# Performance work log

Measured on AMD Instinct MI355X. Metric: run time of the kernel, lower is better.

## Reference

```python
import jax, jax.numpy as jnp
import numpy as np

N = 50000
E = 400000
IN_DIM = 128
HID = 128
OUT = 128
HEADS = 4
NEG_SLOPE = 0.2
EPS = 1e-16


def setup_inputs() -> dict:
    key = jax.random.key(0)
    ks = jax.random.split(key, 12)
    s = 0.05
    return {
        "x": jax.random.normal(ks[0], (N, IN_DIM), dtype=jnp.float32),
        "edge_index": jax.random.randint(ks[1], (2, E), 0, N, dtype=jnp.int64),
        # layer 1: in_dim -> hid, heads=4, concat
        "W1": jax.random.normal(ks[2], (IN_DIM, HEADS * HID), dtype=jnp.float32) * s,
        "att_src1": jax.random.normal(ks[3], (HEADS, HID), dtype=jnp.float32) * s,
        "att_dst1": jax.random.normal(ks[4], (HEADS, HID), dtype=jnp.float32) * s,
        "bias1": jnp.zeros((HEADS * HID,), dtype=jnp.float32),
        # layer 2: hid*heads -> out, heads=1, no concat
        "W2": jax.random.normal(ks[5], (HEADS * HID, OUT), dtype=jnp.float32) * s,
        "att_src2": jax.random.normal(ks[6], (1, OUT), dtype=jnp.float32) * s,
        "att_dst2": jax.random.normal(ks[7], (1, OUT), dtype=jnp.float32) * s,
        "bias2": jnp.zeros((OUT,), dtype=jnp.float32),
    }


def gat_conv(x, src, dst, W, att_src, att_dst, bias, heads, out_dim, concat):
    n = x.shape[0]
    h = (x @ W).reshape(n, heads, out_dim)                       # [N,H,D]
    a_src = jnp.sum(h * att_src[None], axis=-1)                  # [N,H]
    a_dst = jnp.sum(h * att_dst[None], axis=-1)                  # [N,H]
    e = jax.nn.leaky_relu(a_src[src] + a_dst[dst], NEG_SLOPE)    # [E,H]
    # segment softmax over incoming edges of each dst node
    e_max = jax.ops.segment_max(e, dst, num_segments=n)          # [N,H]
    ex = jnp.exp(e - e_max[dst])
    denom = jax.ops.segment_sum(ex, dst, num_segments=n)         # [N,H]
    alpha = ex / (denom[dst] + EPS)                              # [E,H]
    msg = h[src] * alpha[..., None]                              # [E,H,D]
    out = jax.ops.segment_sum(msg, dst, num_segments=n)          # [N,H,D]
    out = out.reshape(n, heads * out_dim) if concat else out.mean(axis=1)
    return out + bias


def reference(x, edge_index, W1, att_src1, att_dst1, bias1, W2, att_src2, att_dst2, bias2):
    n = x.shape[0]
    loop = jnp.arange(n, dtype=edge_index.dtype)
    src = jnp.concatenate([edge_index[0], loop])  # PyG add_self_loops=True
    dst = jnp.concatenate([edge_index[1], loop])
    h = jax.nn.elu(gat_conv(x, src, dst, W1, att_src1, att_dst1, bias1, HEADS, HID, True))
    z = jax.nn.elu(gat_conv(h, src, dst, W2, att_src2, att_dst2, bias2, 1, OUT, False))
    # F.normalize(z, dim=-1): L2 with eps=1e-12 clamp on the norm
    norm = jnp.maximum(jnp.linalg.norm(z, axis=-1, keepdims=True), 1e-12)
    return z / norm
```

## Files before the change

kernel.cpp:

```cpp
#include <hip/hip_runtime.h>
#include <cstddef>

#define N_NODES 50000
#define N_EDGES 400000
#define TOT_EDGES (N_EDGES + N_NODES)
#define M_PAD 50048
#define SCAN_PAD 50176
#define NBLK 49

typedef _Float16 f16;
typedef __attribute__((ext_vector_type(8))) _Float16 f16x8;
typedef __attribute__((ext_vector_type(4))) _Float16 f16x4;
typedef __attribute__((ext_vector_type(2))) _Float16 f16x2;
typedef __attribute__((ext_vector_type(4))) float f32x4;

__global__ void zero_int(int* __restrict__ p, int n) {
  int i = blockIdx.x * blockDim.x + threadIdx.x;
  if (i < n) p[i] = 0;
}

__global__ void count_kernel(const int* __restrict__ ei, int* __restrict__ deg) {
  int e = blockIdx.x * blockDim.x + threadIdx.x;
  if (e >= TOT_EDGES) return;
  int dst = (e < N_EDGES) ? ei[N_EDGES + e] : (e - N_EDGES);
  atomicAdd(&deg[dst], 1);
}

__global__ __launch_bounds__(256) void blk_hist(const int* __restrict__ deg,
                                                int* __restrict__ blkcnt) {
  __shared__ int lh[128];
  const int t = threadIdx.x;
  if (t < 128) lh[t] = 0;
  __syncthreads();
  const int base = blockIdx.x * 1024;
#pragma unroll
  for (int j = 0; j < 4; ++j) {
    const int i = base + j * 256 + t;
    if (i < N_NODES) atomicAdd(&lh[min(deg[i], 127)], 1);
  }
  __syncthreads();
  if (t < 128) blkcnt[t * NBLK + blockIdx.x] = lh[t];
}

__global__ __launch_bounds__(128) void sort_scan(const int* __restrict__ blkcnt,
                                                 int* __restrict__ boff) {
  __shared__ int tot[128];
  const int t = threadIdx.x;
  int s = 0;
  for (int k = 0; k < NBLK; ++k) s += blkcnt[t * NBLK + k];
  tot[t] = s;
  __syncthreads();
  if (t == 0) {
    int acc = 0;
    for (int b = 0; b < 128; ++b) { const int v = tot[b]; tot[b] = acc; acc += v; }
  }
  __syncthreads();
  int acc = tot[t];
  for (int k = 0; k < NBLK; ++k) {
    const int v = blkcnt[t * NBLK + k];
    boff[t * NBLK + k] = acc;
    acc += v;
  }
}

__global__ __launch_bounds__(256) void scatter2(const int* __restrict__ deg,
                                                const int* __restrict__ boff,
                                                int* __restrict__ order) {
  __shared__ int lcur[128];
  const int t = threadIdx.x;
  if (t < 128) lcur[t] = boff[t * NBLK + blockIdx.x];
  __syncthreads();
  const int base = blockIdx.x * 1024;
#pragma unroll
  for (int j = 0; j < 4; ++j) {
    const int i = base + j * 256 + t;
    if (i < N_NODES) {
      const int b = min(deg[i], 127);
      const int pos = atomicAdd(&lcur[b], 1);
      order[pos] = i;
    }
  }
}

__global__ __launch_bounds__(256) void block_scan(const int* __restrict__ cnt,
                                                  int* __restrict__ pre,
                                                  int* __restrict__ bsum) {
  __shared__ int wsum[4];
  const int t = threadIdx.x, lane = t & 63, w = t >> 6;
  const int base = blockIdx.x * 1024 + t * 4;
  int4 v = *(const int4*)&cnt[base];
  const int s = v.x + v.y + v.z + v.w;
  int x = s;
#pragma unroll
  for (int off = 1; off < 64; off <<= 1) {
    int y = __shfl_up(x, off);
    if (lane >= off) x += y;
  }
  if (lane == 63) wsum[w] = x;
  __syncthreads();
  int woff = 0;
  for (int j = 0; j < w; ++j) woff += wsum[j];
  const int ex = x - s + woff;
  pre[base + 0] = ex;
  pre[base + 1] = ex + v.x;
  pre[base + 2] = ex + v.x + v.y;
  pre[base + 3] = ex + v.x + v.y + v.z;
  if (t == 255) bsum[blockIdx.x] = ex + s;
}

__global__ void bsum_scan(int* __restrict__ bsum, int nb) {
  const int lane = threadIdx.x;
  int v = (lane < nb) ? bsum[lane] : 0;
  int x = v;
#pragma unroll
  for (int off = 1; off < 64; off <<= 1) {
    int y = __shfl_up(x, off);
    if (lane >= off) x += y;
  }
  if (lane < nb) bsum[lane] = x - v;
}

__global__ __launch_bounds__(256) void add_off(int* __restrict__ pre,
                                               const int* __restrict__ boff,
                                               int* __restrict__ cursor) {
  const int base = blockIdx.x * 1024 + threadIdx.x * 4;
  const int off = boff[blockIdx.x];
  int4 v = *(const int4*)&pre[base];
  v.x += off; v.y += off; v.z += off; v.w += off;
  *(int4*)&pre[base] = v;
  *(int4*)&cursor[base] = v;
}

__global__ void fill_kernel(const int* __restrict__ ei, int* __restrict__ cursor,
                            int* __restrict__ csr_src) {
  int e = blockIdx.x * blockDim.x + threadIdx.x;
  if (e >= TOT_EDGES) return;
  int s, d;
  if (e < N_EDGES) { s = ei[e]; d = ei[N_EDGES + e]; }
  else             { s = d = e - N_EDGES; }
  int pos = atomicAdd(&cursor[d], 1);
  csr_src[pos] = s;
}

__global__ __launch_bounds__(256) void prep_x(const float* __restrict__ x,
                                              f16* __restrict__ xb,
                                              const float* __restrict__ V1s,
                                              const float* __restrict__ V1d,
                                              float* __restrict__ as1,
                                              float* __restrict__ ad1,
                                              f16* __restrict__ aggb) {
  const int wid = (blockIdx.x * 256 + threadIdx.x) >> 6;
  const int lane = threadIdx.x & 63;
  if (wid >= M_PAD) return;
  const int k = lane * 2;
  if (wid >= N_NODES) {
    f16x2 z; z[0] = (f16)0.f; z[1] = (f16)0.f;
    *(f16x2*)&xb[(size_t)wid * 128 + k] = z;
    f16x8 z8;
#pragma unroll
    for (int j = 0; j < 8; ++j) z8[j] = (f16)0.f;
    *(f16x8*)&aggb[(size_t)wid * 512 + lane * 8] = z8;
    return;
  }
  float2 xv = *(const float2*)&x[(size_t)wid * 128 + k];
  f16x2 o; o[0] = (f16)xv.x; o[1] = (f16)xv.y;
  *(f16x2*)&xb[(size_t)wid * 128 + k] = o;

  float4 vs0 = *(const float4*)&V1s[k * 4];
  float4 vs1 = *(const float4*)&V1s[(k + 1) * 4];
  float4 vd0 = *(const float4*)&V1d[k * 4];
  float4 vd1 = *(const float4*)&V1d[(k + 1) * 4];
  float s[4], d[4];
  s[0] = xv.x * vs0.x + xv.y * vs1.x;
  s[1] = xv.x * vs0.y + xv.y * vs1.y;
  s[2] = xv.x * vs0.z + xv.y * vs1.z;
  s[3] = xv.x * vs0.w + xv.y * vs1.w;
  d[0] = xv.x * vd0.x + xv.y * vd1.x;
  d[1] = xv.x * vd0.y + xv.y * vd1.y;
  d[2] = xv.x * vd0.z + xv.y * vd1.z;
  d[3] = xv.x * vd0.w + xv.y * vd1.w;
#pragma unroll
  for (int h = 0; h < 4; ++h) {
#pragma unroll
    for (int off = 32; off; off >>= 1) {
      s[h] += __shfl_xor(s[h], off);
      d[h] += __shfl_xor(d[h], off);
    }
  }
  if (lane == 0) {
    *(float4*)&as1[(size_t)wid * 4] = make_float4(s[0], s[1], s[2], s[3]);
    *(float4*)&ad1[(size_t)wid * 4] = make_float4(d[0], d[1], d[2], d[3]);
  }
}

__global__ __launch_bounds__(256) void prep_weights(
    const float* __restrict__ W1, const float* __restrict__ W2,
    const float* __restrict__ att_s1, const float* __restrict__ att_d1,
    const float* __restrict__ att_s2, const float* __restrict__ att_d2,
    f16* __restrict__ w1t, f16* __restrict__ w2t,
    float* __restrict__ V1s, float* __restrict__ V1d,
    float* __restrict__ V2s, float* __restrict__ V2d) {
  const int b = blockIdx.x;
  if (b < 256) {
    const int idx = b * 256 + threadIdx.x;
    const int cc = idx >> 7, rr = idx & 127;
    w1t[idx] = (f16)W1[(size_t)rr * 512 + cc];
  } else if (b < 512) {
    const int idx = (b - 256) * 256 + threadIdx.x;
    const int cc = idx >> 9, rr = idx & 511;
    w2t[idx] = (f16)W2[(size_t)rr * 128 + cc];
  } else if (b < 640) {
    const int wid = (b - 512) * 4 + (threadIdx.x >> 6);
    const int lane = threadIdx.x & 63;
    const int k = wid >> 2, h = wid & 3;
    const float* wrow = W1 + (size_t)k * 512 + h * 128;
    float2 wv = *(const float2*)&wrow[lane * 2];
    float2 sv = *(const float2*)&att_s1[h * 128 + lane * 2];
    float2 dv = *(const float2*)&att_d1[h * 128 + lane * 2];
    float ps = wv.x * sv.x + wv.y * sv.y;
    float pd = wv.x * dv.x + wv.y * dv.y;
#pragma unroll
    for (int off = 32; off; off >>= 1) {
      ps += __shfl_xor(ps, off);
      pd += __shfl_xor(pd, off);
    }
    if (lane == 0) { V1s[k * 4 + h] = ps; V1d[k * 4 + h] = pd; }
  } else {
    const int wid = (b - 640) * 4 + (threadIdx.x >> 6);
    const int lane = threadIdx.x & 63;
    const float* wrow = W2 + (size_t)wid * 128;
    float2 wv = *(const float2*)&wrow[lane * 2];
    float2 sv = *(const float2*)&att_s2[lane * 2];
    float2 dv = *(const float2*)&att_d2[lane * 2];
    float ps = wv.x * sv.x + wv.y * sv.y;
    float pd = wv.x * dv.x + wv.y * dv.y;
#pragma unroll
    for (int off = 32; off; off >>= 1) {
      ps += __shfl_xor(ps, off);
      pd += __shfl_xor(pd, off);
    }
    if (lane == 0) { V2s[wid] = ps; V2d[wid] = pd; }
  }
}

template <int K, bool PER_HEAD, bool FUSE_A2>
__global__ __launch_bounds__(256) void gemm_bt(const f16* __restrict__ A, int lda,
                                               const f16* __restrict__ Bt, int ldb,
                                               f16* __restrict__ C, int ldc,
                                               const float* __restrict__ bias,
                                               const float* __restrict__ V2s,
                                               const float* __restrict__ V2d,
                                               float* __restrict__ as2,
                                               float* __restrict__ ad2) {
  if constexpr (PER_HEAD) {
    const int hh = blockIdx.y;
    A += (size_t)hh * 128;
    Bt += (size_t)hh * 128 * 128;
    C += (size_t)hh * 128;
    bias += hh * 128;
  }
  constexpr int LDT = 40;
  __shared__ __align__(16) f16 As[128 * LDT];
  __shared__ __align__(16) f16 Bs[128 * LDT];
  const int tid = threadIdx.x;
  const int lane = tid & 63;
  const int g = lane >> 4, r16 = lane & 15;
  const int w = tid >> 6, wr = w >> 1, wc = w & 1;
  const long bm = (long)blockIdx.x * 128;

  const int row0 = tid >> 2, h0 = tid & 3;
  const int p1 = (h0 & 1) * 16 + (h0 >> 1) * 4;
  const size_t ga0 = (size_t)(bm + row0) * lda + h0 * 8;
  const size_t ga1 = (size_t)(bm + row0 + 64) * lda + h0 * 8;
  const size_t gb0 = (size_t)row0 * ldb + h0 * 8;
  const size_t gb1 = (size_t)(row0 + 64) * ldb + h0 * 8;
  const int la0 = row0 * LDT + p1, la1 = (row0 + 64) * LDT + p1;

  f32x4 acc[4][4] = {};
  float s2a = 0.f, d2a = 0.f, s2b = 0.f, d2b = 0.f;

  for (int k0 = 0; k0 < K; k0 += 32) {
    __syncthreads();
    f16x8 va0 = *(const f16x8*)&A[ga0 + k0];
    f16x8 va1 = *(const f16x8*)&A[ga1 + k0];
    f16x8 vb0 = *(const f16x8*)&Bt[gb0 + k0];
    f16x8 vb1 = *(const f16x8*)&Bt[gb1 + k0];
    if constexpr (FUSE_A2) {
      const int kc = k0 + h0 * 8;
      float4 vsa = *(const float4*)&V2s[kc];
      float4 vsb = *(const float4*)&V2s[kc + 4];
      float4 vda = *(const float4*)&V2d[kc];
      float4 vdb = *(const float4*)&V2d[kc + 4];
      const float vs[8] = {vsa.x, vsa.y, vsa.z, vsa.w, vsb.x, vsb.y, vsb.z, vsb.w};
      const float vd[8] = {vda.x, vda.y, vda.z, vda.w, vdb.x, vdb.y, vdb.z, vdb.w};
#pragma unroll
      for (int j = 0; j < 8; ++j) {
        s2a += (float)va0[j] * vs[j];
        d2a += (float)va0[j] * vd[j];
        s2b += (float)va1[j] * vs[j];
        d2b += (float)va1[j] * vd[j];
      }
    }
    *(f16x4*)&As[la0]     = __builtin_shufflevector(va0, va0, 0, 1, 2, 3);
    *(f16x4*)&As[la0 + 8] = __builtin_shufflevector(va0, va0, 4, 5, 6, 7);
    *(f16x4*)&As[la1]     = __builtin_shufflevector(va1, va1, 0, 1, 2, 3);
    *(f16x4*)&As[la1 + 8] = __builtin_shufflevector(va1, va1, 4, 5, 6, 7);
    *(f16x4*)&Bs[la0]     = __builtin_shufflevector(vb0, vb0, 0, 1, 2, 3);
    *(f16x4*)&Bs[la0 + 8] = __builtin_shufflevector(vb0, vb0, 4, 5, 6, 7);
    *(f16x4*)&Bs[la1]     = __builtin_shufflevector(vb1, vb1, 0, 1, 2, 3);
    *(f16x4*)&Bs[la1 + 8] = __builtin_shufflevector(vb1, vb1, 4, 5, 6, 7);
    __syncthreads();
    f16x8 af[4], bfv[4];
#pragma unroll
    for (int m = 0; m < 4; ++m)
      af[m] = *(const f16x8*)&As[(wr * 64 + m * 16 + r16) * LDT + g * 8];
#pragma unroll
    for (int n = 0; n < 4; ++n)
      bfv[n] = *(const f16x8*)&Bs[(wc * 64 + n * 16 + r16) * LDT + g * 8];
#pragma unroll
    for (int m = 0; m < 4; ++m)
#pragma unroll
      for (int n = 0; n < 4; ++n)
        acc[m][n] = __builtin_amdgcn_mfma_f32_16x16x32_f16(af[m], bfv[n], acc[m][n], 0, 0, 0);
  }

  if constexpr (FUSE_A2) {
    s2a += __shfl_xor(s2a, 1); s2a += __shfl_xor(s2a, 2);
    d2a += __shfl_xor(d2a, 1); d2a += __shfl_xor(d2a, 2);
    s2b += __shfl_xor(s2b, 1); s2b += __shfl_xor(s2b, 2);
    d2b += __shfl_xor(d2b, 1); d2b += __shfl_xor(d2b, 2);
    if ((tid & 3) == 0) {
      const long r0 = bm + row0;
      as2[r0] = s2a; ad2[r0] = d2a;
      as2[r0 + 64] = s2b; ad2[r0 + 64] = d2b;
    }
  }

#pragma unroll
  for (int m = 0; m < 4; ++m) {
#pragma unroll
    for (int n = 0; n < 4; ++n) {
      const long row = bm + wr * 64 + m * 16 + g * 4;
      const int col = wc * 64 + n * 16 + r16;
      float bv = 0.f;
      if constexpr (PER_HEAD) bv = bias[col];
#pragma unroll
      for (int r = 0; r < 4; ++r) {
        float v = acc[m][n][r];
        if constexpr (PER_HEAD) {
          v += bv;
          v = v > 0.f ? v : (__expf(v) - 1.f);
        }
        C[(size_t)(row + r) * ldc + col] = (f16)v;
      }
    }
  }
}

__global__ __launch_bounds__(256) void aggregate1x(
    const f16* __restrict__ xsrc, const float* __restrict__ a_src,
    const float* __restrict__ a_dst, const int* __restrict__ rowstart,
    const int* __restrict__ csr, const int* __restrict__ order,
    f16* __restrict__ aggb) {
  const int wave = (blockIdx.x * blockDim.x + threadIdx.x) >> 6;
  const int lane = threadIdx.x & 63;
  const int g16 = lane >> 4, l16 = lane & 15;
  const int node = order[wave * 4 + g16];
  const int col0 = l16 * 8;
  const int rs = rowstart[node];
  const int re = rowstart[node + 1];
  const int deg = re - rs;
  float4 adv = *(const float4*)&a_dst[(size_t)node * 4];

  int maxdeg = deg;
  maxdeg = max(maxdeg, __shfl_xor(maxdeg, 16));
  maxdeg = max(maxdeg, __shfl_xor(maxdeg, 32));

  constexpr int D = 4;
  int sreg[D];
  float4 areg[D];
  f16x8 hreg[D];
#pragma unroll
  for (int p = 0; p < D; ++p) {
    const int k = rs + p;
    const int s = csr[(k < re) ? k : (re - 1)];
    areg[p] = *(const float4*)&a_src[(size_t)s * 4];
    hreg[p] = *(const f16x8*)&xsrc[(size_t)s * 128 + col0];
    const int k2 = rs + D + p;
    sreg[p] = csr[(k2 < re) ? k2 : (re - 1)];
  }

  float acc0[8] = {}, acc1[8] = {}, acc2[8] = {}, acc3[8] = {};
  float Z0 = 0.f, Z1 = 0.f, Z2 = 0.f, Z3 = 0.f;
  for (int base = 0; base < maxdeg; base += D) {
#pragma unroll
    for (int p = 0; p < D; ++p) {
      const int i = base + p;
      const bool act = i < deg;
      float4 av = areg[p];
      float e0 = av.x + adv.x; e0 = e0 > 0.f ? e0 : 0.2f * e0;
      float e1 = av.y + adv.y; e1 = e1 > 0.f ? e1 : 0.2f * e1;
      float e2 = av.z + adv.z; e2 = e2 > 0.f ? e2 : 0.2f * e2;
      float e3 = av.w + adv.w; e3 = e3 > 0.f ? e3 : 0.2f * e3;
      const float w0 = act ? __expf(e0) : 0.f;
      const float w1 = act ? __expf(e1) : 0.f;
      const float w2 = act ? __expf(e2) : 0.f;
      const float w3 = act ? __expf(e3) : 0.f;
      const f16x8 h = hreg[p];
      const int nk = rs + i + D;
      if (nk < re) {
        const int s = sreg[p];
        areg[p] = *(const float4*)&a_src[(size_t)s * 4];
        hreg[p] = *(const f16x8*)&xsrc[(size_t)s * 128 + col0];
      }
      const int nk2 = rs + i + 2 * D;
      if (nk2 < re) sreg[p] = csr[nk2];
      Z0 += w0; Z1 += w1; Z2 += w2; Z3 += w3;
#pragma unroll
      for (int j = 0; j < 8; ++j) {
        const float hv = (float)h[j];
        acc0[j] += w0 * hv;
        acc1[j] += w1 * hv;
        acc2[j] += w2 * hv;
        acc3[j] += w3 * hv;
      }
    }
  }

  const float i0 = 1.f / (Z0 + 1e-16f);
  const float i1 = 1.f / (Z1 + 1e-16f);
  const float i2 = 1.f / (Z2 + 1e-16f);
  const float i3 = 1.f / (Z3 + 1e-16f);
  f16* orow = aggb + (size_t)node * 512 + col0;
  f16x8 o0, o1, o2, o3;
#pragma unroll
  for (int j = 0; j < 8; ++j) {
    o0[j] = (f16)(acc0[j] * i0);
    o1[j] = (f16)(acc1[j] * i1);
    o2[j] = (f16)(acc2[j] * i2);
    o3[j] = (f16)(acc3[j] * i3);
  }
  *(f16x8*)&orow[0]   = o0;
  *(f16x8*)&orow[128] = o1;
  *(f16x8*)&orow[256] = o2;
  *(f16x8*)&orow[384] = o3;
}

__global__ __launch_bounds__(256) void aggregate2(
    const f16* __restrict__ hsrc, const float* __restrict__ a_src,
    const float* __restrict__ a_dst, const int* __restrict__ rowstart,
    const int* __restrict__ csr, const int* __restrict__ order,
    const float* __restrict__ bias, float* __restrict__ out) {
  const int wave = (blockIdx.x * blockDim.x + threadIdx.x) >> 6;
  const int lane = threadIdx.x & 63;
  const int g16 = lane >> 4, l16 = lane & 15;
  const int node = order[wave * 4 + g16];
  const int col0 = l16 * 8;
  const int rs = rowstart[node];
  const int re = rowstart[node + 1];
  const int deg = re - rs;
  const float ad = a_dst[node];

  int maxdeg = deg;
  maxdeg = max(maxdeg, __shfl_xor(maxdeg, 16));
  maxdeg = max(maxdeg, __shfl_xor(maxdeg, 32));

  constexpr int D = 6;
  int sreg[D];
  float areg[D];
  f16x8 hreg[D];
#pragma unroll
  for (int p = 0; p < D; ++p) {
    const int k = rs + p;
    const int s = csr[(k < re) ? k : (re - 1)];
    areg[p] = a_src[s];
    hreg[p] = *(const f16x8*)&hsrc[(size_t)s * 128 + col0];
    const int k2 = rs + D + p;
    sreg[p] = csr[(k2 < re) ? k2 : (re - 1)];
  }

  float acc[8] = {};
  float Z = 0.f;
  for (int base = 0; base < maxdeg; base += D) {
#pragma unroll
    for (int p = 0; p < D; ++p) {
      const int i = base + p;
      const bool act = i < deg;
      float e = areg[p] + ad;
      e = e > 0.f ? e : 0.2f * e;
      const float w = act ? __expf(e) : 0.f;
      const f16x8 h = hreg[p];
      const int nk = rs + i + D;
      if (nk < re) {
        const int s = sreg[p];
        areg[p] = a_src[s];
        hreg[p] = *(const f16x8*)&hsrc[(size_t)s * 128 + col0];
      }
      const int nk2 = rs + i + 2 * D;
      if (nk2 < re) sreg[p] = csr[nk2];
      Z += w;
#pragma unroll
      for (int j = 0; j < 8; ++j) acc[j] += w * (float)h[j];
    }
  }
  const float inv = 1.f / (Z + 1e-16f);

  float4 ba = *(const float4*)&bias[col0];
  float4 bb = *(const float4*)&bias[col0 + 4];
  const float bv[8] = {ba.x, ba.y, ba.z, ba.w, bb.x, bb.y, bb.z, bb.w};
  float v[8];
  float ss = 0.f;
#pragma unroll
  for (int j = 0; j < 8; ++j) {
    float t = acc[j] * inv + bv[j];
    t = t > 0.f ? t : (__expf(t) - 1.f);
    v[j] = t;
    ss += t * t;
  }
  ss += __shfl_xor(ss, 1);
  ss += __shfl_xor(ss, 2);
  ss += __shfl_xor(ss, 4);
  ss += __shfl_xor(ss, 8);
  const float invn = 1.f / fmaxf(sqrtf(ss), 1e-12f);
  float* orow = out + (size_t)node * 128 + col0;
  float4 oa = make_float4(v[0] * invn, v[1] * invn, v[2] * invn, v[3] * invn);
  float4 ob = make_float4(v[4] * invn, v[5] * invn, v[6] * invn, v[7] * invn);
  *(float4*)&orow[0] = oa;
  *(float4*)&orow[4] = ob;
}

extern "C" void kernel_launch(void* const* d_in, const int* in_sizes, int n_in,
                              void* d_out, int out_size, void* d_ws, size_t ws_size,
                              hipStream_t stream) {
  const float* x        = (const float*)d_in[0];
  const int*   ei       = (const int*)d_in[1];
  const float* W1       = (const float*)d_in[2];
  const float* att_src1 = (const float*)d_in[3];
  const float* att_dst1 = (const float*)d_in[4];
  const float* bias1    = (const float*)d_in[5];
  const float* W2       = (const float*)d_in[6];
  const float* att_src2 = (const float*)d_in[7];
  const float* att_dst2 = (const float*)d_in[8];
  const float* bias2    = (const float*)d_in[9];
  float* out = (float*)d_out;

  char* ws = (char*)d_ws;
  size_t off = 0;
  auto alloc = [&](size_t bytes) {
    char* p = ws + off;
    off = (off + bytes + 255) & ~(size_t)255;
    return p;
  };
  f16* xb    = (f16*)alloc(sizeof(f16) * (size_t)M_PAD * 128);
  f16* w1t   = (f16*)alloc(sizeof(f16) * 512 * 128);
  f16* w2t   = (f16*)alloc(sizeof(f16) * 128 * 512);
  f16* aggb  = (f16*)alloc(sizeof(f16) * (size_t)M_PAD * 512);
  f16* out1b = (f16*)alloc(sizeof(f16) * (size_t)M_PAD * 512);
  float* V1s = (float*)alloc(sizeof(float) * 512);
  float* V1d = (float*)alloc(sizeof(float) * 512);
  float* V2s = (float*)alloc(sizeof(float) * 512);
  float* V2d = (float*)alloc(sizeof(float) * 512);
  float* as1 = (float*)alloc(sizeof(float) * N_NODES * 4);
  float* ad1 = (float*)alloc(sizeof(float) * N_NODES * 4);
  float* as2 = (float*)alloc(sizeof(float) * M_PAD);
  float* ad2 = (float*)alloc(sizeof(float) * M_PAD);
  int* rowstart = (int*)alloc(sizeof(int) * (SCAN_PAD + 4));
  int* deg      = (int*)alloc(sizeof(int) * SCAN_PAD);
  int* cursor   = (int*)alloc(sizeof(int) * SCAN_PAD);
  int* bsum     = (int*)alloc(sizeof(int) * 64);
  int* blkcnt   = (int*)alloc(sizeof(int) * 128 * NBLK);
  int* boff     = (int*)alloc(sizeof(int) * 128 * NBLK);
  int* order    = (int*)alloc(sizeof(int) * N_NODES);
  int* csr      = (int*)alloc(sizeof(int) * TOT_EDGES);
  f16* h2b = aggb;

  const int wgridP = (M_PAD * 64) / 256;
  const int agrid  = (N_NODES / 4) * 64 / 256;

  zero_int<<<(SCAN_PAD + 255) / 256, 256, 0, stream>>>(deg, SCAN_PAD);
  count_kernel<<<(TOT_EDGES + 255) / 256, 256, 0, stream>>>(ei, deg);
  blk_hist<<<NBLK, 256, 0, stream>>>(deg, blkcnt);
  block_scan<<<NBLK, 256, 0, stream>>>(deg, rowstart, bsum);
  bsum_scan<<<1, 64, 0, stream>>>(bsum, NBLK);
  sort_scan<<<1, 128, 0, stream>>>(blkcnt, boff);
  add_off<<<NBLK, 256, 0, stream>>>(rowstart, bsum, cursor);
  scatter2<<<NBLK, 256, 0, stream>>>(deg, boff, order);
  fill_kernel<<<(TOT_EDGES + 255) / 256, 256, 0, stream>>>(ei, cursor, csr);

  prep_weights<<<768, 256, 0, stream>>>(W1, W2, att_src1, att_dst1,
                                        att_src2, att_dst2, w1t, w2t,
                                        V1s, V1d, V2s, V2d);
  prep_x<<<wgridP, 256, 0, stream>>>(x, xb, V1s, V1d, as1, ad1, aggb);

  aggregate1x<<<agrid, 256, 0, stream>>>(xb, as1, ad1, rowstart, csr, order, aggb);
  gemm_bt<128, true, false><<<dim3(M_PAD / 128, 4), 256, 0, stream>>>(
      aggb, 512, w1t, 128, out1b, 512, bias1, nullptr, nullptr, nullptr, nullptr);

  gemm_bt<512, false, true><<<dim3(M_PAD / 128, 1), 256, 0, stream>>>(
      out1b, 512, w2t, 512, h2b, 128, nullptr, V2s, V2d, as2, ad2);
  aggregate2<<<agrid, 256, 0, stream>>>(h2b, as2, ad2, rowstart, csr, order, bias2, out);
}
```

Before: 200.5 us.

## Merge preprocessing kernels and precompute per-edge attention weights in CSR order

Cuts the preprocessing chain from about eleven launches to five by merging degree counting with weight prep, histogram/scan with x conversion, the two small scans, and add-offset with scatter. Per-edge exp(leaky_relu) attention weights are now computed once in edge-parallel kernels: during CSR fill for layer 1, and in a new edge_w2 kernel after the second GEMM for layer 2. The aggregation kernels then stream these precomputed weights instead of gathering a_src and evaluating exp inside the wave loop. This removes launch overhead and per-lane transcendental work, at the cost of extra global traffic for the weight arrays and csrd, plus one added kernel launch.

```diff
diff --git a/kernel.cpp b/kernel.cpp
--- a/kernel.cpp
+++ b/kernel.cpp
@@ -7,6 +7,7 @@
 #define M_PAD 50048
 #define SCAN_PAD 50176
 #define NBLK 49
+#define CNT_BLKS 1758
 
 typedef _Float16 f16;
 typedef __attribute__((ext_vector_type(8))) _Float16 f16x8;
@@ -14,144 +15,113 @@
 typedef __attribute__((ext_vector_type(2))) _Float16 f16x2;
 typedef __attribute__((ext_vector_type(4))) float f32x4;
 
+__device__ __forceinline__ float lrelu(float e) { return e > 0.f ? e : 0.2f * e; }
+
 __global__ void zero_int(int* __restrict__ p, int n) {
   int i = blockIdx.x * blockDim.x + threadIdx.x;
   if (i < n) p[i] = 0;
 }
 
-__global__ void count_kernel(const int* __restrict__ ei, int* __restrict__ deg) {
-  int e = blockIdx.x * blockDim.x + threadIdx.x;
-  if (e >= TOT_EDGES) return;
-  int dst = (e < N_EDGES) ? ei[N_EDGES + e] : (e - N_EDGES);
-  atomicAdd(&deg[dst], 1);
-}
-
-__global__ __launch_bounds__(256) void blk_hist(const int* __restrict__ deg,
-                                                int* __restrict__ blkcnt) {
+__global__ __launch_bounds__(256) void count_weights(
+    const int* __restrict__ ei, int* __restrict__ deg,
+    const float* __restrict__ W1, const float* __restrict__ W2,
+    const float* __restrict__ att_s1, const float* __restrict__ att_d1,
+    const float* __restrict__ att_s2, const float* __restrict__ att_d2,
+    f16* __restrict__ w1t, f16* __restrict__ w2t,
+    float* __restrict__ V1s, float* __restrict__ V1d,
+    float* __restrict__ V2s, float* __restrict__ V2d) {
+  const int b = blockIdx.x;
+  if (b < CNT_BLKS) {
+    const int e = b * 256 + threadIdx.x;
+    if (e >= TOT_EDGES) return;
+    const int dst = (e < N_EDGES) ? ei[N_EDGES + e] : (e - N_EDGES);
+    atomicAdd(&deg[dst], 1);
+    return;
+  }
+  const int bb = b - CNT_BLKS;
+  if (bb < 256) {
+    const int idx = bb * 256 + threadIdx.x;
+    const int cc = idx >> 7, rr = idx & 127;
+    w1t[idx] = (f16)W1[(size_t)rr * 512 + cc];
+  } else if (bb < 512) {
+    const int idx = (bb - 256) * 256 + threadIdx.x;
+    const int cc = idx >> 9, rr = idx & 511;
+    w2t[idx] = (f16)W2[(size_t)rr * 128 + cc];
+  } else if (bb < 640) {
+    const int wid = (bb - 512) * 4 + (threadIdx.x >> 6);
+    const int lane = threadIdx.x & 63;
+    const int k = wid >> 2, h = wid & 3;
+    const float* wrow = W1 + (size_t)k * 512 + h * 128;
+    float2 wv = *(const float2*)&wrow[lane * 2];
+    float2 sv = *(const float2*)&att_s1[h * 128 + lane * 2];
+    float2 dv = *(const float2*)&att_d1[h * 128 + lane * 2];
+    float ps = wv.x * sv.x + wv.y * sv.y;
+    float pd = wv.x * dv.x + wv.y * dv.y;
+#pragma unroll
+    for (int off = 32; off; off >>= 1) {
+      ps += __shfl_xor(ps, off);
+      pd += __shfl_xor(pd, off);
+    }
+    if (lane == 0) { V1s[k * 4 + h] = ps; V1d[k * 4 + h] = pd; }
+  } else {
+    const int wid = (bb - 640) * 4 + (threadIdx.x >> 6);
+    const int lane = threadIdx.x & 63;
+    const float* wrow = W2 + (size_t)wid * 128;
+    float2 wv = *(const float2*)&wrow[lane * 2];
+    float2 sv = *(const float2*)&att_s2[lane * 2];
+    float2 dv = *(const float2*)&att_d2[lane * 2];
+    float ps = wv.x * sv.x + wv.y * sv.y;
+    float pd = wv.x * dv.x + wv.y * dv.y;
+#pragma unroll
+    for (int off = 32; off; off >>= 1) {
+      ps += __shfl_xor(ps, off);
+      pd += __shfl_xor(pd, off);
+    }
+    if (lane == 0) { V2s[wid] = ps; V2d[wid] = pd; }
+  }
+}
+
+__global__ __launch_bounds__(256) void histscan_prepx(
+    const int* __restrict__ deg, int* __restrict__ pre, int* __restrict__ bsum,
+    int* __restrict__ blkcnt,
+    const float* __restrict__ x, f16* __restrict__ xb,
+    const float* __restrict__ V1s, const float* __restrict__ V1d,
+    float* __restrict__ as1, float* __restrict__ ad1, f16* __restrict__ aggb) {
+  __shared__ int wsum[4];
   __shared__ int lh[128];
-  const int t = threadIdx.x;
-  if (t < 128) lh[t] = 0;
-  __syncthreads();
-  const int base = blockIdx.x * 1024;
-#pragma unroll
-  for (int j = 0; j < 4; ++j) {
-    const int i = base + j * 256 + t;
-    if (i < N_NODES) atomicAdd(&lh[min(deg[i], 127)], 1);
-  }
-  __syncthreads();
-  if (t < 128) blkcnt[t * NBLK + blockIdx.x] = lh[t];
-}
-
-__global__ __launch_bounds__(128) void sort_scan(const int* __restrict__ blkcnt,
-                                                 int* __restrict__ boff) {
-  __shared__ int tot[128];
-  const int t = threadIdx.x;
-  int s = 0;
-  for (int k = 0; k < NBLK; ++k) s += blkcnt[t * NBLK + k];
-  tot[t] = s;
-  __syncthreads();
-  if (t == 0) {
-    int acc = 0;
-    for (int b = 0; b < 128; ++b) { const int v = tot[b]; tot[b] = acc; acc += v; }
-  }
-  __syncthreads();
-  int acc = tot[t];
-  for (int k = 0; k < NBLK; ++k) {
-    const int v = blkcnt[t * NBLK + k];
-    boff[t * NBLK + k] = acc;
-    acc += v;
-  }
-}
-
-__global__ __launch_bounds__(256) void scatter2(const int* __restrict__ deg,
-                                                const int* __restrict__ boff,
-                                                int* __restrict__ order) {
-  __shared__ int lcur[128];
-  const int t = threadIdx.x;
-  if (t < 128) lcur[t] = boff[t * NBLK + blockIdx.x];
-  __syncthreads();
-  const int base = blockIdx.x * 1024;
-#pragma unroll
-  for (int j = 0; j < 4; ++j) {
-    const int i = base + j * 256 + t;
-    if (i < N_NODES) {
-      const int b = min(deg[i], 127);
-      const int pos = atomicAdd(&lcur[b], 1);
-      order[pos] = i;
-    }
-  }
-}
-
-__global__ __launch_bounds__(256) void block_scan(const int* __restrict__ cnt,
-                                                  int* __restrict__ pre,
-                                                  int* __restrict__ bsum) {
-  __shared__ int wsum[4];
-  const int t = threadIdx.x, lane = t & 63, w = t >> 6;
-  const int base = blockIdx.x * 1024 + t * 4;
-  int4 v = *(const int4*)&cnt[base];
-  const int s = v.x + v.y + v.z + v.w;
-  int x = s;
-#pragma unroll
-  for (int off = 1; off < 64; off <<= 1) {
-    int y = __shfl_up(x, off);
-    if (lane >= off) x += y;
-  }
-  if (lane == 63) wsum[w] = x;
-  __syncthreads();
-  int woff = 0;
-  for (int j = 0; j < w; ++j) woff += wsum[j];
-  const int ex = x - s + woff;
-  pre[base + 0] = ex;
-  pre[base + 1] = ex + v.x;
-  pre[base + 2] = ex + v.x + v.y;
-  pre[base + 3] = ex + v.x + v.y + v.z;
-  if (t == 255) bsum[blockIdx.x] = ex + s;
-}
-
-__global__ void bsum_scan(int* __restrict__ bsum, int nb) {
-  const int lane = threadIdx.x;
-  int v = (lane < nb) ? bsum[lane] : 0;
-  int x = v;
-#pragma unroll
-  for (int off = 1; off < 64; off <<= 1) {
-    int y = __shfl_up(x, off);
-    if (lane >= off) x += y;
-  }
-  if (lane < nb) bsum[lane] = x - v;
-}
-
-__global__ __launch_bounds__(256) void add_off(int* __restrict__ pre,
-                                               const int* __restrict__ boff,
-                                               int* __restrict__ cursor) {
-  const int base = blockIdx.x * 1024 + threadIdx.x * 4;
-  const int off = boff[blockIdx.x];
-  int4 v = *(const int4*)&pre[base];
-  v.x += off; v.y += off; v.z += off; v.w += off;
-  *(int4*)&pre[base] = v;
-  *(int4*)&cursor[base] = v;
-}
-
-__global__ void fill_kernel(const int* __restrict__ ei, int* __restrict__ cursor,
-                            int* __restrict__ csr_src) {
-  int e = blockIdx.x * blockDim.x + threadIdx.x;
-  if (e >= TOT_EDGES) return;
-  int s, d;
-  if (e < N_EDGES) { s = ei[e]; d = ei[N_EDGES + e]; }
-  else             { s = d = e - N_EDGES; }
-  int pos = atomicAdd(&cursor[d], 1);
-  csr_src[pos] = s;
-}
-
-__global__ __launch_bounds__(256) void prep_x(const float* __restrict__ x,
-                                              f16* __restrict__ xb,
-                                              const float* __restrict__ V1s,
-                                              const float* __restrict__ V1d,
-                                              float* __restrict__ as1,
-                                              float* __restrict__ ad1,
-                                              f16* __restrict__ aggb) {
-  const int wid = (blockIdx.x * 256 + threadIdx.x) >> 6;
+  const int b = blockIdx.x;
+  if (b < NBLK) {
+    const int t = threadIdx.x, lane = t & 63, w = t >> 6;
+    if (t < 128) lh[t] = 0;
+    __syncthreads();
+    const int base = b * 1024 + t * 4;
+    int4 v = *(const int4*)&deg[base];
+    if (base + 0 < N_NODES) atomicAdd(&lh[min(v.x, 127)], 1);
+    if (base + 1 < N_NODES) atomicAdd(&lh[min(v.y, 127)], 1);
+    if (base + 2 < N_NODES) atomicAdd(&lh[min(v.z, 127)], 1);
+    if (base + 3 < N_NODES) atomicAdd(&lh[min(v.w, 127)], 1);
+    const int s = v.x + v.y + v.z + v.w;
+    int xx = s;
+#pragma unroll
+    for (int off = 1; off < 64; off <<= 1) {
+      int y = __shfl_up(xx, off);
+      if (lane >= off) xx += y;
+    }
+    if (lane == 63) wsum[w] = xx;
+    __syncthreads();
+    int woff = 0;
+    for (int j = 0; j < w; ++j) woff += wsum[j];
+    const int ex = xx - s + woff;
+    pre[base + 0] = ex;
+    pre[base + 1] = ex + v.x;
+    pre[base + 2] = ex + v.x + v.y;
+    pre[base + 3] = ex + v.x + v.y + v.z;
+    if (t == 255) bsum[b] = ex + s;
+    if (t < 128) blkcnt[t * NBLK + b] = lh[t];
+    return;
+  }
+  const int wid = (b - NBLK) * 4 + (threadIdx.x >> 6);
   const int lane = threadIdx.x & 63;
-  if (wid >= M_PAD) return;
   const int k = lane * 2;
   if (wid >= N_NODES) {
     f16x2 z; z[0] = (f16)0.f; z[1] = (f16)0.f;
@@ -165,7 +135,6 @@
   float2 xv = *(const float2*)&x[(size_t)wid * 128 + k];
   f16x2 o; o[0] = (f16)xv.x; o[1] = (f16)xv.y;
   *(f16x2*)&xb[(size_t)wid * 128 + k] = o;
-
   float4 vs0 = *(const float4*)&V1s[k * 4];
   float4 vs1 = *(const float4*)&V1s[(k + 1) * 4];
   float4 vd0 = *(const float4*)&V1d[k * 4];
@@ -193,54 +162,91 @@
   }
 }
 
-__global__ __launch_bounds__(256) void prep_weights(
-    const float* __restrict__ W1, const float* __restrict__ W2,
-    const float* __restrict__ att_s1, const float* __restrict__ att_d1,
-    const float* __restrict__ att_s2, const float* __restrict__ att_d2,
-    f16* __restrict__ w1t, f16* __restrict__ w2t,
-    float* __restrict__ V1s, float* __restrict__ V1d,
-    float* __restrict__ V2s, float* __restrict__ V2d) {
+__global__ __launch_bounds__(128) void scan2(int* __restrict__ bsum,
+                                             const int* __restrict__ blkcnt,
+                                             int* __restrict__ boff) {
+  __shared__ int tot[128];
+  const int t = threadIdx.x;
+  int s = 0;
+  for (int k = 0; k < NBLK; ++k) s += blkcnt[t * NBLK + k];
+  tot[t] = s;
+  __syncthreads();
+  if (t == 0) {
+    int acc = 0;
+    for (int b = 0; b < 128; ++b) { const int v = tot[b]; tot[b] = acc; acc += v; }
+  }
+  __syncthreads();
+  int acc = tot[t];
+  for (int k = 0; k < NBLK; ++k) {
+    boff[t * NBLK + k] = acc;
+    acc += blkcnt[t * NBLK + k];
+  }
+  if (t < 64) {
+    int v = (t < NBLK) ? bsum[t] : 0;
+    int xx = v;
+#pragma unroll
+    for (int off = 1; off < 64; off <<= 1) {
+      int y = __shfl_up(xx, off);
+      if (t >= off) xx += y;
+    }
+    if (t < NBLK) bsum[t] = xx - v;
+  }
+}
+
+__global__ __launch_bounds__(256) void scatter_addoff(
+    int* __restrict__ pre, const int* __restrict__ bsumoff,
+    int* __restrict__ cursor, const int* __restrict__ deg,
+    const int* __restrict__ boff, int* __restrict__ order) {
+  __shared__ int lcur[128];
+  const int t = threadIdx.x;
   const int b = blockIdx.x;
-  if (b < 256) {
-    const int idx = b * 256 + threadIdx.x;
-    const int cc = idx >> 7, rr = idx & 127;
-    w1t[idx] = (f16)W1[(size_t)rr * 512 + cc];
-  } else if (b < 512) {
-    const int idx = (b - 256) * 256 + threadIdx.x;
-    const int cc = idx >> 9, rr = idx & 511;
-    w2t[idx] = (f16)W2[(size_t)rr * 128 + cc];
-  } else if (b < 640) {
-    const int wid = (b - 512) * 4 + (threadIdx.x >> 6);
-    const int lane = threadIdx.x & 63;
-    const int k = wid >> 2, h = wid & 3;
-    const float* wrow = W1 + (size_t)k * 512 + h * 128;
-    float2 wv = *(const float2*)&wrow[lane * 2];
-    float2 sv = *(const float2*)&att_s1[h * 128 + lane * 2];
-    float2 dv = *(const float2*)&att_d1[h * 128 + lane * 2];
-    float ps = wv.x * sv.x + wv.y * sv.y;
-    float pd = wv.x * dv.x + wv.y * dv.y;
-#pragma unroll
-    for (int off = 32; off; off >>= 1) {
-      ps += __shfl_xor(ps, off);
-      pd += __shfl_xor(pd, off);
-    }
-    if (lane == 0) { V1s[k * 4 + h] = ps; V1d[k * 4 + h] = pd; }
-  } else {
-    const int wid = (b - 640) * 4 + (threadIdx.x >> 6);
-    const int lane = threadIdx.x & 63;
-    const float* wrow = W2 + (size_t)wid * 128;
-    float2 wv = *(const float2*)&wrow[lane * 2];
-    float2 sv = *(const float2*)&att_s2[lane * 2];
-    float2 dv = *(const float2*)&att_d2[lane * 2];
-    float ps = wv.x * sv.x + wv.y * sv.y;
-    float pd = wv.x * dv.x + wv.y * dv.y;
-#pragma unroll
-    for (int off = 32; off; off >>= 1) {
-      ps += __shfl_xor(ps, off);
-      pd += __shfl_xor(pd, off);
-    }
-    if (lane == 0) { V2s[wid] = ps; V2d[wid] = pd; }
-  }
+  if (t < 128) lcur[t] = boff[t * NBLK + b];
+  __syncthreads();
+  const int base4 = b * 1024 + t * 4;
+  const int off = bsumoff[b];
+  int4 v = *(const int4*)&pre[base4];
+  v.x += off; v.y += off; v.z += off; v.w += off;
+  *(int4*)&pre[base4] = v;
+  *(int4*)&cursor[base4] = v;
+#pragma unroll
+  for (int j = 0; j < 4; ++j) {
+    const int i = b * 1024 + j * 256 + t;
+    if (i < N_NODES) {
+      const int bk = min(deg[i], 127);
+      const int pos = atomicAdd(&lcur[bk], 1);
+      order[pos] = i;
+    }
+  }
+}
+
+__global__ void fill_w1(const int* __restrict__ ei, int* __restrict__ cursor,
+                        const float* __restrict__ as1, const float* __restrict__ ad1,
+                        int* __restrict__ csr, int* __restrict__ csrd,
+                        float* __restrict__ wexp1) {
+  const int e = blockIdx.x * blockDim.x + threadIdx.x;
+  if (e >= TOT_EDGES) return;
+  int s, d;
+  if (e < N_EDGES) { s = ei[e]; d = ei[N_EDGES + e]; }
+  else             { s = d = e - N_EDGES; }
+  const int pos = atomicAdd(&cursor[d], 1);
+  csr[pos] = s;
+  csrd[pos] = d;
+  float4 a = *(const float4*)&as1[(size_t)s * 4];
+  float4 bz = *(const float4*)&ad1[(size_t)d * 4];
+  float4 w;
+  w.x = __expf(lrelu(a.x + bz.x));
+  w.y = __expf(lrelu(a.y + bz.y));
+  w.z = __expf(lrelu(a.z + bz.z));
+  w.w = __expf(lrelu(a.w + bz.w));
+  *(float4*)&wexp1[(size_t)pos * 4] = w;
+}
+
+__global__ void edge_w2(const int* __restrict__ csr, const int* __restrict__ csrd,
+                        const float* __restrict__ as2, const float* __restrict__ ad2,
+                        float* __restrict__ w2exp) {
+  const int kk = blockIdx.x * blockDim.x + threadIdx.x;
+  if (kk >= TOT_EDGES) return;
+  w2exp[kk] = __expf(lrelu(as2[csr[kk]] + ad2[csrd[kk]]));
 }
 
 template <int K, bool PER_HEAD, bool FUSE_A2>
@@ -358,10 +364,9 @@
 }
 
 __global__ __launch_bounds__(256) void aggregate1x(
-    const f16* __restrict__ xsrc, const float* __restrict__ a_src,
-    const float* __restrict__ a_dst, const int* __restrict__ rowstart,
-    const int* __restrict__ csr, const int* __restrict__ order,
-    f16* __restrict__ aggb) {
+    const f16* __restrict__ xsrc, const float* __restrict__ wexp,
+    const int* __restrict__ rowstart, const int* __restrict__ csr,
+    const int* __restrict__ order, f16* __restrict__ aggb) {
   const int wave = (blockIdx.x * blockDim.x + threadIdx.x) >> 6;
   const int lane = threadIdx.x & 63;
   const int g16 = lane >> 4, l16 = lane & 15;
@@ -370,7 +375,6 @@
   const int rs = rowstart[node];
   const int re = rowstart[node + 1];
   const int deg = re - rs;
-  float4 adv = *(const float4*)&a_dst[(size_t)node * 4];
 
   int maxdeg = deg;
   maxdeg = max(maxdeg, __shfl_xor(maxdeg, 16));
@@ -378,13 +382,14 @@
 
   constexpr int D = 4;
   int sreg[D];
-  float4 areg[D];
+  float4 wreg[D];
   f16x8 hreg[D];
 #pragma unroll
   for (int p = 0; p < D; ++p) {
     const int k = rs + p;
-    const int s = csr[(k < re) ? k : (re - 1)];
-    areg[p] = *(const float4*)&a_src[(size_t)s * 4];
+    const int kc = (k < re) ? k : (re - 1);
+    wreg[p] = *(const float4*)&wexp[(size_t)kc * 4];
+    const int s = csr[kc];
     hreg[p] = *(const f16x8*)&xsrc[(size_t)s * 128 + col0];
     const int k2 = rs + D + p;
     sreg[p] = csr[(k2 < re) ? k2 : (re - 1)];
@@ -397,20 +402,16 @@
     for (int p = 0; p < D; ++p) {
       const int i = base + p;
       const bool act = i < deg;
-      float4 av = areg[p];
-      float e0 = av.x + adv.x; e0 = e0 > 0.f ? e0 : 0.2f * e0;
-      float e1 = av.y + adv.y; e1 = e1 > 0.f ? e1 : 0.2f * e1;
-      float e2 = av.z + adv.z; e2 = e2 > 0.f ? e2 : 0.2f * e2;
-      float e3 = av.w + adv.w; e3 = e3 > 0.f ? e3 : 0.2f * e3;
-      const float w0 = act ? __expf(e0) : 0.f;
-      const float w1 = act ? __expf(e1) : 0.f;
-      const float w2 = act ? __expf(e2) : 0.f;
-      const float w3 = act ? __expf(e3) : 0.f;
+      float4 wv = wreg[p];
+      const float w0 = act ? wv.x : 0.f;
+      const float w1 = act ? wv.y : 0.f;
+      const float w2 = act ? wv.z : 0.f;
+      const float w3 = act ? wv.w : 0.f;
       const f16x8 h = hreg[p];
       const int nk = rs + i + D;
       if (nk < re) {
+        wreg[p] = *(const float4*)&wexp[(size_t)nk * 4];
         const int s = sreg[p];
-        areg[p] = *(const float4*)&a_src[(size_t)s * 4];
         hreg[p] = *(const f16x8*)&xsrc[(size_t)s * 128 + col0];
       }
       const int nk2 = rs + i + 2 * D;
@@ -447,10 +448,10 @@
 }
 
 __global__ __launch_bounds__(256) void aggregate2(
-    const f16* __restrict__ hsrc, const float* __restrict__ a_src,
-    const float* __restrict__ a_dst, const int* __restrict__ rowstart,
-    const int* __restrict__ csr, const int* __restrict__ order,
-    const float* __restrict__ bias, float* __restrict__ out) {
+    const f16* __restrict__ hsrc, const float* __restrict__ w2exp,
+    const int* __restrict__ rowstart, const int* __restrict__ csr,
+    const int* __restrict__ order, const float* __restrict__ bias,
+    float* __restrict__ out) {
   const int wave = (blockIdx.x * blockDim.x + threadIdx.x) >> 6;
   const int lane = threadIdx.x & 63;
   const int g16 = lane >> 4, l16 = lane & 15;
@@ -459,7 +460,6 @@
   const int rs = rowstart[node];
   const int re = rowstart[node + 1];
   const int deg = re - rs;
-  const float ad = a_dst[node];
 
   int maxdeg = deg;
   maxdeg = max(maxdeg, __shfl_xor(maxdeg, 16));
@@ -467,13 +467,14 @@
 
   constexpr int D = 6;
   int sreg[D];
-  float areg[D];
+  float wreg[D];
   f16x8 hreg[D];
 #pragma unroll
   for (int p = 0; p < D; ++p) {
     const int k = rs + p;
-    const int s = csr[(k < re) ? k : (re - 1)];
-    areg[p] = a_src[s];
+    const int kc = (k < re) ? k : (re - 1);
+    wreg[p] = w2exp[kc];
+    const int s = csr[kc];
     hreg[p] = *(const f16x8*)&hsrc[(size_t)s * 128 + col0];
     const int k2 = rs + D + p;
     sreg[p] = csr[(k2 < re) ? k2 : (re - 1)];
@@ -486,14 +487,12 @@
     for (int p = 0; p < D; ++p) {
       const int i = base + p;
       const bool act = i < deg;
-      float e = areg[p] + ad;
-      e = e > 0.f ? e : 0.2f * e;
-      const float w = act ? __expf(e) : 0.f;
+      const float w = act ? wreg[p] : 0.f;
       const f16x8 h = hreg[p];
       const int nk = rs + i + D;
       if (nk < re) {
+        wreg[p] = w2exp[nk];
         const int s = sreg[p];
-        areg[p] = a_src[s];
         hreg[p] = *(const f16x8*)&hsrc[(size_t)s * 128 + col0];
       }
       const int nk2 = rs + i + 2 * D;
@@ -564,6 +563,8 @@
   float* ad1 = (float*)alloc(sizeof(float) * N_NODES * 4);
   float* as2 = (float*)alloc(sizeof(float) * M_PAD);
   float* ad2 = (float*)alloc(sizeof(float) * M_PAD);
+  float* wexp1 = (float*)alloc(sizeof(float) * (size_t)TOT_EDGES * 4);
+  float* w2exp = (float*)alloc(sizeof(float) * TOT_EDGES);
   int* rowstart = (int*)alloc(sizeof(int) * (SCAN_PAD + 4));
   int* deg      = (int*)alloc(sizeof(int) * SCAN_PAD);
   int* cursor   = (int*)alloc(sizeof(int) * SCAN_PAD);
@@ -572,31 +573,25 @@
   int* boff     = (int*)alloc(sizeof(int) * 128 * NBLK);
   int* order    = (int*)alloc(sizeof(int) * N_NODES);
   int* csr      = (int*)alloc(sizeof(int) * TOT_EDGES);
+  int* csrd     = (int*)alloc(sizeof(int) * TOT_EDGES);
   f16* h2b = aggb;
 
-  const int wgridP = (M_PAD * 64) / 256;
-  const int agrid  = (N_NODES / 4) * 64 / 256;
+  const int agrid = (N_NODES / 4) * 64 / 256;
 
   zero_int<<<(SCAN_PAD + 255) / 256, 256, 0, stream>>>(deg, SCAN_PAD);
-  count_kernel<<<(TOT_EDGES + 255) / 256, 256, 0, stream>>>(ei, deg);
-  blk_hist<<<NBLK, 256, 0, stream>>>(deg, blkcnt);
-  block_scan<<<NBLK, 256, 0, stream>>>(deg, rowstart, bsum);
-  bsum_scan<<<1, 64, 0, stream>>>(bsum, NBLK);
-  sort_scan<<<1, 128, 0, stream>>>(blkcnt, boff);
-  add_off<<<NBLK, 256, 0, stream>>>(rowstart, bsum, cursor);
-  scatter2<<<NBLK, 256, 0, stream>>>(deg, boff, order);
-  fill_kernel<<<(TOT_EDGES + 255) / 256, 256, 0, stream>>>(ei, cursor, csr);
-
-  prep_weights<<<768, 256, 0, stream>>>(W1, W2, att_src1, att_dst1,
-                                        att_src2, att_dst2, w1t, w2t,
-                                        V1s, V1d, V2s, V2d);
-  prep_x<<<wgridP, 256, 0, stream>>>(x, xb, V1s, V1d, as1, ad1, aggb);
-
-  aggregate1x<<<agrid, 256, 0, stream>>>(xb, as1, ad1, rowstart, csr, order, aggb);
+  count_weights<<<CNT_BLKS + 768, 256, 0, stream>>>(
+      ei, deg, W1, W2, att_src1, att_dst1, att_src2, att_dst2,
+      w1t, w2t, V1s, V1d, V2s, V2d);
+  histscan_prepx<<<NBLK + M_PAD / 4, 256, 0, stream>>>(
+      deg, rowstart, bsum, blkcnt, x, xb, V1s, V1d, as1, ad1, aggb);
+  scan2<<<1, 128, 0, stream>>>(bsum, blkcnt, boff);
+  scatter_addoff<<<NBLK, 256, 0, stream>>>(rowstart, bsum, cursor, deg, boff, order);
+  fill_w1<<<CNT_BLKS, 256, 0, stream>>>(ei, cursor, as1, ad1, csr, csrd, wexp1);
+  aggregate1x<<<agrid, 256, 0, stream>>>(xb, wexp1, rowstart, csr, order, aggb);
   gemm_bt<128, true, false><<<dim3(M_PAD / 128, 4), 256, 0, stream>>>(
       aggb, 512, w1t, 128, out1b, 512, bias1, nullptr, nullptr, nullptr, nullptr);
-
   gemm_bt<512, false, true><<<dim3(M_PAD / 128, 1), 256, 0, stream>>>(
       out1b, 512, w2t, 512, h2b, 128, nullptr, V2s, V2d, as2, ad2);
-  aggregate2<<<agrid, 256, 0, stream>>>(h2b, as2, ad2, rowstart, csr, order, bias2, out);
-}
+  edge_w2<<<CNT_BLKS, 256, 0, stream>>>(csr, csrd, as2, ad2, w2exp);
+  aggregate2<<<agrid, 256, 0, stream>>>(h2b, w2exp, rowstart, csr, order, bias2, out);
+}
```

Result: no change. 199.7 us (-0.4%).
